# Optimization experiments

Hardware: AMD Instinct MI355X
Metric: run time of the kernel (lower is better)

Reference implementation:

```python
import jax, jax.numpy as jnp
import numpy as np

V, D, S, L, H = 32000, 768, 1024, 6, 12
HS = D // H
EPS = 1e-5


def setup_inputs() -> dict:
    key = jax.random.key(0)
    ks = jax.random.split(key, 20)
    std = 0.02
    inp = {
        "idx": jax.random.randint(ks[0], (4, 1024), 0, V),
        "tok_emb": jax.random.normal(ks[1], (V, D), jnp.float32) * std,
        "pos_emb": jax.random.normal(ks[2], (S, D), jnp.float32) * std,
        "Wq": jax.random.normal(ks[3], (L, H, D, HS), jnp.float32) * std,
        "Wk": jax.random.normal(ks[4], (L, H, D, HS), jnp.float32) * std,
        "Wv": jax.random.normal(ks[5], (L, H, D, HS), jnp.float32) * std,
        "Wp": jax.random.normal(ks[6], (L, D, D), jnp.float32) * std,
        "bp": jnp.zeros((L, D), jnp.float32),
        "ln1g": jnp.ones((L, D), jnp.float32),
        "ln1b": jnp.zeros((L, D), jnp.float32),
        "ln2g": jnp.ones((L, D), jnp.float32),
        "ln2b": jnp.zeros((L, D), jnp.float32),
        "W1": jax.random.normal(ks[7], (L, D, 4 * D), jnp.float32) * std,
        "b1": jnp.zeros((L, 4 * D), jnp.float32),
        "W2": jax.random.normal(ks[8], (L, 4 * D, D), jnp.float32) * std,
        "b2": jnp.zeros((L, D), jnp.float32),
        "lnfg": jnp.ones((D,), jnp.float32),
        "lnfb": jnp.zeros((D,), jnp.float32),
        "lmW": jax.random.normal(ks[9], (D, V), jnp.float32) * std,
        "lmb": jnp.zeros((V,), jnp.float32),
    }
    return inp


def _layernorm(x, g, b):
    m = jnp.mean(x, axis=-1, keepdims=True)
    v = jnp.mean(jnp.square(x - m), axis=-1, keepdims=True)
    return (x - m) * jax.lax.rsqrt(v + EPS) * g + b


def _gpt_forward(idx, tok_emb, pos_emb, Wq, Wk, Wv, Wp, bp,
                 ln1g, ln1b, ln2g, ln2b, W1, b1, W2, b2,
                 lnfg, lnfb, lmW, lmb):
    B, T = idx.shape
    x = tok_emb[idx] + pos_emb[:T]              # [B,T,D]
    tril = jnp.tril(jnp.ones((T, T), bool))
    scale = HS ** -0.5
    for l in range(L):
        h = _layernorm(x, ln1g[l], ln1b[l])
        q = jnp.einsum('btd,hdk->bhtk', h, Wq[l])
        k = jnp.einsum('btd,hdk->bhtk', h, Wk[l])
        v = jnp.einsum('btd,hdk->bhtk', h, Wv[l])
        att = jnp.einsum('bhtk,bhsk->bhts', q, k) * scale
        att = jnp.where(tril, att, -jnp.inf)
        att = jax.nn.softmax(att, axis=-1)
        o = jnp.einsum('bhts,bhsk->bhtk', att, v)          # [B,H,T,HS]
        o = o.transpose(0, 2, 1, 3).reshape(B, T, D)       # concat heads
        x = x + o @ Wp[l] + bp[l]
        h2 = _layernorm(x, ln2g[l], ln2b[l])
        x = x + jax.nn.relu(h2 @ W1[l] + b1[l]) @ W2[l] + b2[l]
    x = _layernorm(x, lnfg, lnfb)
    logits = x @ lmW + lmb                                  # [B,T,V]
    return logits


def reference(idx, tok_emb, pos_emb, Wq, Wk, Wv, Wp, bp,
              ln1g, ln1b, ln2g, ln2b, W1, b1, W2, b2,
              lnfg, lnfb, lmW, lmb):
    return _gpt_forward(idx, tok_emb, pos_emb, Wq, Wk, Wv, Wp, bp,
                        ln1g, ln1b, ln2g, ln2b, W1, b1, W2, b2,
                        lnfg, lnfb, lmW, lmb)
```

## Files before the change

### kernel.cpp

```cpp
#include <hip/hip_runtime.h>
#include <hip/hip_bf16.h>
#include <cstdint>
#include <cstddef>


typedef __bf16 bf16x8 __attribute__((ext_vector_type(8)));
typedef __bf16 bf16x4 __attribute__((ext_vector_type(4)));
typedef float  f32x4  __attribute__((ext_vector_type(4)));

#define MFMA16(a, b, c) __builtin_amdgcn_mfma_f32_16x16x32_bf16((a), (b), (c), 0, 0, 0)

__device__ __forceinline__ void g2l16(const void* g, void* l) {
    __builtin_amdgcn_global_load_lds(
        (const __attribute__((address_space(1))) void*)g,
        (__attribute__((address_space(3))) void*)l, 16, 0, 0);
}

__global__ __launch_bounds__(256) void transpose_cvt(
    const float* __restrict__ src, __bf16* __restrict__ dst,
    int K, int N, int nNT)
{
    const float* s = src + (size_t)blockIdx.y * K * N;
    __bf16*      d = dst + (size_t)blockIdx.y * K * N;
    int kt = blockIdx.x / nNT, nt = blockIdx.x % nNT;
    int k0 = kt * 32, n0 = nt * 32;
    __shared__ float t[32][33];
    int tx = threadIdx.x & 31, ty = threadIdx.x >> 5;
#pragma unroll
    for (int i = 0; i < 4; i++)
        t[ty + i * 8][tx] = s[(size_t)(k0 + ty + i * 8) * N + n0 + tx];
    __syncthreads();
#pragma unroll
    for (int i = 0; i < 4; i++)
        d[(size_t)(n0 + ty + i * 8) * K + k0 + tx] = (__bf16)t[tx][ty + i * 8];
}

__global__ __launch_bounds__(256) void repack_qkv(
    const float* __restrict__ Wq, const float* __restrict__ Wk,
    const float* __restrict__ Wv, __bf16* __restrict__ dst)
{
    int l = blockIdx.z;
    int m = blockIdx.y / 12, h = blockIdx.y % 12;
    int kt = blockIdx.x / 2, nt = blockIdx.x % 2;
    const float* W = (m == 0 ? Wq : (m == 1 ? Wk : Wv)) + ((size_t)(l * 12 + h)) * 768 * 64;
    __bf16* d = dst + (size_t)l * 2304 * 768 + (size_t)(m * 768 + h * 64) * 768;
    int k0 = kt * 32, n0 = nt * 32;
    __shared__ float t[32][33];
    int tx = threadIdx.x & 31, ty = threadIdx.x >> 5;
#pragma unroll
    for (int i = 0; i < 4; i++)
        t[ty + i * 8][tx] = W[(size_t)(k0 + ty + i * 8) * 64 + n0 + tx];
    __syncthreads();
#pragma unroll
    for (int i = 0; i < 4; i++)
        d[(size_t)(n0 + ty + i * 8) * 768 + k0 + tx] = (__bf16)t[tx][ty + i * 8];
}

__global__ __launch_bounds__(256) void embed_kernel(
    const int* __restrict__ idx, const float* __restrict__ tok,
    const float* __restrict__ pos, float* __restrict__ x)
{
    const int t = blockIdx.x, tid = threadIdx.x;
    int id = idx[t];
    const float* te = tok + (size_t)id * 768;
    const float* pe = pos + (size_t)(t & 1023) * 768;
    float* xr = x + (size_t)t * 768;
    xr[tid]       = te[tid]       + pe[tid];
    xr[tid + 256] = te[tid + 256] + pe[tid + 256];
    xr[tid + 512] = te[tid + 512] + pe[tid + 512];
}

__global__ __launch_bounds__(256) void ln_kernel(
    const float* __restrict__ x, const float* __restrict__ g,
    const float* __restrict__ bb, __bf16* __restrict__ out)
{
    const int row = blockIdx.x, tid = threadIdx.x;
    const float* xr = x + (size_t)row * 768;
    float v0 = xr[tid], v1 = xr[tid + 256], v2 = xr[tid + 512];
    float s  = v0 + v1 + v2;
    float s2 = v0 * v0 + v1 * v1 + v2 * v2;
#pragma unroll
    for (int d = 1; d < 64; d <<= 1) {
        s  += __shfl_xor(s, d);
        s2 += __shfl_xor(s2, d);
    }
    __shared__ float sb[8];
    int w = tid >> 6, l = tid & 63;
    if (l == 0) { sb[w] = s; sb[4 + w] = s2; }
    __syncthreads();
    s  = sb[0] + sb[1] + sb[2] + sb[3];
    s2 = sb[4] + sb[5] + sb[6] + sb[7];
    float mean = s * (1.f / 768.f);
    float var  = s2 * (1.f / 768.f) - mean * mean;
    float rstd = rsqrtf(var + 1e-5f);
    __bf16* orow = out + (size_t)row * 768;
    orow[tid]       = (__bf16)((v0 - mean) * rstd * g[tid]       + bb[tid]);
    orow[tid + 256] = (__bf16)((v1 - mean) * rstd * g[tid + 256] + bb[tid + 256]);
    orow[tid + 512] = (__bf16)((v2 - mean) * rstd * g[tid + 512] + bb[tid + 512]);
}

template <int RELU, int BIAS, int RES, int OBF16, int VT>
__global__ __launch_bounds__(256, 4) void gemm_bt(
    const __bf16* __restrict__ A, const __bf16* __restrict__ Bt,
    const float* __restrict__ bias, const float* __restrict__ res,
    void* __restrict__ Cout, __bf16* __restrict__ vt, int M, int N, int K)
{
    __shared__ __bf16 As[128 * 64];
    __shared__ __bf16 Bs[128 * 64];
    const int tid = threadIdx.x;
    const int w = tid >> 6, lane = tid & 63, lr = lane & 15, lg = lane >> 4;
    const int wr = w >> 1, wc = w & 1;

    const int MT  = gridDim.y;
    const int nwg = gridDim.x * gridDim.y;
    const int ord = blockIdx.y * gridDim.x + blockIdx.x;
    const int qq = nwg >> 3, rm = nwg & 7;
    const int xcd = ord & 7, pos = ord >> 3;
    const int wgid = (xcd < rm ? xcd * (qq + 1) : rm * (qq + 1) + (xcd - rm) * qq) + pos;
    const int m0 = (wgid % MT) * 128, n0 = (wgid / MT) * 128;

    f32x4 acc[4][4];
#pragma unroll
    for (int i = 0; i < 4; i++)
#pragma unroll
        for (int j = 0; j < 4; j++) acc[i][j] = (f32x4){0.f, 0.f, 0.f, 0.f};

    const __bf16* Abase = A  + (size_t)m0 * K;
    const __bf16* Bbase = Bt + (size_t)n0 * K;

    for (int k0 = 0; k0 < K; k0 += 64) {
#pragma unroll
        for (int u = 0; u < 4; ++u) {
            int chunk = u * 256 + tid;
            int rr = chunk >> 3, cc = chunk & 7;
            int se = (cc ^ (rr & 7)) << 3;
            g2l16(Abase + (size_t)rr * K + k0 + se, (char*)As + chunk * 16);
            g2l16(Bbase + (size_t)rr * K + k0 + se, (char*)Bs + chunk * 16);
        }
        __syncthreads();
#pragma unroll
        for (int ks = 0; ks < 2; ++ks) {
            bf16x8 af[4], bfv[4];
#pragma unroll
            for (int i = 0; i < 4; ++i) {
                int ra = wr * 64 + i * 16 + lr;
                af[i]  = *(const bf16x8*)((const char*)As + ra * 128 + (((ks * 4 + lg) ^ (ra & 7)) << 4));
                int rb = wc * 64 + i * 16 + lr;
                bfv[i] = *(const bf16x8*)((const char*)Bs + rb * 128 + (((ks * 4 + lg) ^ (rb & 7)) << 4));
            }
#pragma unroll
            for (int i = 0; i < 4; ++i)
#pragma unroll
                for (int j = 0; j < 4; ++j)
                    acc[i][j] = MFMA16(af[i], bfv[j], acc[i][j]);
        }
        __syncthreads();
    }

    const bool isv = VT && (n0 >= 1536);
#pragma unroll
    for (int i = 0; i < 4; i++) {
        int row = m0 + wr * 64 + i * 16 + lg * 4;
#pragma unroll
        for (int j = 0; j < 4; j++) {
            int col = n0 + wc * 64 + j * 16 + lr;
            if (isv) {
                int bb = row >> 10, tl = row & 1023;
                int vrow = (bb * 12 + ((col - 1536) >> 6)) * 64 + (col & 63);
                bf16x4 pv;
#pragma unroll
                for (int rr = 0; rr < 4; ++rr) pv[rr] = (__bf16)(acc[i][j][rr]);
                *(bf16x4*)&vt[(size_t)vrow * 1024 + tl] = pv;
            } else {
                float bv = BIAS ? bias[col] : 0.f;
#pragma unroll
                for (int rr = 0; rr < 4; rr++) {
                    float v = acc[i][j][rr] + bv;
                    if (RES)  v += res[(size_t)(row + rr) * N + col];
                    if (RELU) v = fmaxf(v, 0.f);
                    if (OBF16) ((__bf16*)Cout)[(size_t)(row + rr) * N + col] = (__bf16)v;
                    else       ((float*)Cout)[(size_t)(row + rr) * N + col] = v;
                }
            }
        }
    }
}

__global__ __launch_bounds__(256, 3) void attn_kernel(
    const __bf16* __restrict__ qkv, const __bf16* __restrict__ vt,
    __bf16* __restrict__ o)
{
    __shared__ __bf16 Kl[128 * 64];
    __shared__ __bf16 Vl[64 * 128];
    __shared__ __bf16 Pl[4][16][72];
    const int qb = blockIdx.x, h = blockIdx.y, b = blockIdx.z;
    const int tid = threadIdx.x, w = tid >> 6, lane = tid & 63, lr = lane & 15, lg = lane >> 4;
    const int q0 = qb * 64 + w * 16;
    const size_t rowb = (size_t)b * 1024;
    const __bf16* Kg = qkv + rowb * 2304 + 768 + (size_t)h * 64;
    const __bf16* Vg = vt + (size_t)(b * 12 + h) * 64 * 1024;

    bf16x8 qf[2];
    {
        const __bf16* qp = qkv + (rowb + q0 + lr) * 2304 + h * 64 + lg * 8;
        qf[0] = *(const bf16x8*)qp;
        qf[1] = *(const bf16x8*)(qp + 32);
    }

    f32x4 oacc[4];
#pragma unroll
    for (int i = 0; i < 4; i++) oacc[i] = (f32x4){0.f, 0.f, 0.f, 0.f};
    float lpart[4] = {0.f, 0.f, 0.f, 0.f};

    const int nkb = (qb >> 1) + 1;
    for (int kb = 0; kb < nkb; ++kb) {
        __syncthreads();
#pragma unroll
        for (int u = 0; u < 4; ++u) {
            int chunk = u * 256 + tid;
            int kr = chunk >> 3, cc = chunk & 7;
            g2l16(Kg + (size_t)(kb * 128 + kr) * 2304 + ((cc ^ (kr & 7)) << 3),
                  (char*)Kl + chunk * 16);
        }
#pragma unroll
        for (int u = 0; u < 4; ++u) {
            int chunk = u * 256 + tid;
            int vr = chunk >> 4, cc = chunk & 15;
            g2l16(Vg + (size_t)vr * 1024 + kb * 128 + ((cc ^ (vr & 15)) << 3),
                  (char*)Vl + chunk * 16);
        }
        __syncthreads();

#pragma unroll
        for (int hh = 0; hh < 2; ++hh) {
            if (kb * 128 + hh * 64 > q0 + 15) break;
            float e[4][4];
#pragma unroll
            for (int cb = 0; cb < 4; ++cb) {
                const int krow = hh * 64 + cb * 16 + lr;
                const int key  = kb * 128 + krow;
                bf16x8 k0 = *(const bf16x8*)((const char*)Kl + krow * 128 + ((lg ^ (krow & 7)) << 4));
                bf16x8 k1 = *(const bf16x8*)((const char*)Kl + krow * 128 + (((4 + lg) ^ (krow & 7)) << 4));
                f32x4 s = (f32x4){0.f, 0.f, 0.f, 0.f};
                s = MFMA16(qf[0], k0, s);
                s = MFMA16(qf[1], k1, s);
#pragma unroll
                for (int rr = 0; rr < 4; rr++) {
                    int qrow = q0 + lg * 4 + rr;
                    float p = (key > qrow) ? -1e30f : s[rr] * 0.125f;
                    e[cb][rr] = __expf(p - 3.0f);
                }
            }
#pragma unroll
            for (int rr = 0; rr < 4; rr++) {
                lpart[rr] += (e[0][rr] + e[1][rr]) + (e[2][rr] + e[3][rr]);
                Pl[w][lg * 4 + rr][lr]      = (__bf16)e[0][rr];
                Pl[w][lg * 4 + rr][16 + lr] = (__bf16)e[1][rr];
                Pl[w][lg * 4 + rr][32 + lr] = (__bf16)e[2][rr];
                Pl[w][lg * 4 + rr][48 + lr] = (__bf16)e[3][rr];
            }
            bf16x8 pf0 = *(const bf16x8*)&Pl[w][lr][lg * 8];
            bf16x8 pf1 = *(const bf16x8*)&Pl[w][lr][32 + lg * 8];
#pragma unroll
            for (int nb = 0; nb < 4; nb++) {
                const int vrow = nb * 16 + lr;
                bf16x8 v0 = *(const bf16x8*)((const char*)Vl + vrow * 256 + (((hh * 8 + lg) ^ (vrow & 15)) << 4));
                bf16x8 v1 = *(const bf16x8*)((const char*)Vl + vrow * 256 + (((hh * 8 + 4 + lg) ^ (vrow & 15)) << 4));
                oacc[nb] = MFMA16(pf0, v0, oacc[nb]);
                oacc[nb] = MFMA16(pf1, v1, oacc[nb]);
            }
        }
    }

#pragma unroll
    for (int rr = 0; rr < 4; rr++) {
        float ls = lpart[rr];
        ls += __shfl_xor(ls, 1);
        ls += __shfl_xor(ls, 2);
        ls += __shfl_xor(ls, 4);
        ls += __shfl_xor(ls, 8);
        float inv = 1.0f / ls;
        size_t row = rowb + q0 + lg * 4 + rr;
#pragma unroll
        for (int nb = 0; nb < 4; nb++)
            o[row * 768 + h * 64 + nb * 16 + lr] = (__bf16)(oacc[nb][rr] * inv);
    }
}

extern "C" void kernel_launch(void* const* d_in, const int* in_sizes, int n_in,
                              void* d_out, int out_size, void* d_ws, size_t ws_size,
                              hipStream_t stream)
{
    (void)in_sizes; (void)n_in; (void)out_size; (void)ws_size;
    const int*   idx  = (const int*)d_in[0];
    const float* tok  = (const float*)d_in[1];
    const float* pos  = (const float*)d_in[2];
    const float* Wq   = (const float*)d_in[3];
    const float* Wk   = (const float*)d_in[4];
    const float* Wv   = (const float*)d_in[5];
    const float* Wp   = (const float*)d_in[6];
    const float* bp   = (const float*)d_in[7];
    const float* ln1g = (const float*)d_in[8];
    const float* ln1b = (const float*)d_in[9];
    const float* ln2g = (const float*)d_in[10];
    const float* ln2b = (const float*)d_in[11];
    const float* W1   = (const float*)d_in[12];
    const float* b1   = (const float*)d_in[13];
    const float* W2   = (const float*)d_in[14];
    const float* b2   = (const float*)d_in[15];
    const float* lnfg = (const float*)d_in[16];
    const float* lnfb = (const float*)d_in[17];
    const float* lmW  = (const float*)d_in[18];
    const float* lmb  = (const float*)d_in[19];

    char* ws = (char*)d_ws;
    size_t off = 0;
    auto alloc = [&](size_t bytes) {
        char* p = ws + off;
        off += (bytes + 255) & ~(size_t)255;
        return p;
    };
    __bf16* Wqkv_t = (__bf16*)alloc((size_t)6 * 2304 * 768 * 2);
    __bf16* Wp_t   = (__bf16*)alloc((size_t)6 * 768 * 768 * 2);
    __bf16* W1_t   = (__bf16*)alloc((size_t)6 * 3072 * 768 * 2);
    __bf16* W2_t   = (__bf16*)alloc((size_t)6 * 768 * 3072 * 2);
    __bf16* lm_t   = (__bf16*)alloc((size_t)32000 * 768 * 2);
    float*  x      = (float*)alloc((size_t)4096 * 768 * 4);
    __bf16* hbuf   = (__bf16*)alloc((size_t)4096 * 768 * 2);
    __bf16* qkv    = (__bf16*)alloc((size_t)4096 * 2304 * 2);
    __bf16* obuf   = (__bf16*)alloc((size_t)4096 * 768 * 2);
    __bf16* mlp    = (__bf16*)alloc((size_t)4096 * 3072 * 2);
    __bf16* vt     = mlp;

    transpose_cvt<<<dim3(24 * 24, 6), 256, 0, stream>>>(Wp, Wp_t, 768, 768, 24);
    transpose_cvt<<<dim3(24 * 96, 6), 256, 0, stream>>>(W1, W1_t, 768, 3072, 96);
    transpose_cvt<<<dim3(96 * 24, 6), 256, 0, stream>>>(W2, W2_t, 3072, 768, 24);
    transpose_cvt<<<dim3(24 * 1000, 1), 256, 0, stream>>>(lmW, lm_t, 768, 32000, 1000);
    repack_qkv<<<dim3(48, 36, 6), 256, 0, stream>>>(Wq, Wk, Wv, Wqkv_t);

    embed_kernel<<<4096, 256, 0, stream>>>(idx, tok, pos, x);

    for (int l = 0; l < 6; l++) {
        ln_kernel<<<4096, 256, 0, stream>>>(x, ln1g + l * 768, ln1b + l * 768, hbuf);
        gemm_bt<0, 0, 0, 1, 1><<<dim3(18, 32), 256, 0, stream>>>(
            hbuf, Wqkv_t + (size_t)l * 2304 * 768, nullptr, nullptr, qkv, vt, 4096, 2304, 768);
        attn_kernel<<<dim3(16, 12, 4), 256, 0, stream>>>(qkv, vt, obuf);
        gemm_bt<0, 1, 1, 0, 0><<<dim3(6, 32), 256, 0, stream>>>(
            obuf, Wp_t + (size_t)l * 768 * 768, bp + l * 768, x, x, nullptr, 4096, 768, 768);
        ln_kernel<<<4096, 256, 0, stream>>>(x, ln2g + l * 768, ln2b + l * 768, hbuf);
        gemm_bt<1, 1, 0, 1, 0><<<dim3(24, 32), 256, 0, stream>>>(
            hbuf, W1_t + (size_t)l * 3072 * 768, b1 + l * 3072, nullptr, mlp, nullptr, 4096, 3072, 768);
        gemm_bt<0, 1, 1, 0, 0><<<dim3(6, 32), 256, 0, stream>>>(
            mlp, W2_t + (size_t)l * 768 * 3072, b2 + l * 768, x, x, nullptr, 4096, 768, 3072);
    }

    ln_kernel<<<4096, 256, 0, stream>>>(x, lnfg, lnfb, hbuf);
    gemm_bt<0, 1, 0, 0, 0><<<dim3(250, 32), 256, 0, stream>>>(
        hbuf, lm_t, lmb, nullptr, d_out, nullptr, 4096, 32000, 768);
}
```

Measured before the change: 1.512 ms.

## Vectorize transposes/embed/layernorm and add 256x128-tile LM-head GEMM

The weight transpose and repack kernels now read float4 and write bf16x4. Embedding and layernorm process one row per wavefront with vectorized loads, which removes the shared-memory reduction and barrier in layernorm. A new 512-thread LM-head GEMM uses 256x128 tiles with 8 waves, doubling A-tile reuse for the largest matmul. The larger tiles raise LDS and register use per block, which may reduce occupancy.

```diff
diff --git a/kernel.cpp b/kernel.cpp
--- a/kernel.cpp
+++ b/kernel.cpp
@@ -25,14 +25,15 @@
     int kt = blockIdx.x / nNT, nt = blockIdx.x % nNT;
     int k0 = kt * 32, n0 = nt * 32;
     __shared__ float t[32][33];
-    int tx = threadIdx.x & 31, ty = threadIdx.x >> 5;
-#pragma unroll
-    for (int i = 0; i < 4; i++)
-        t[ty + i * 8][tx] = s[(size_t)(k0 + ty + i * 8) * N + n0 + tx];
+    int rr = threadIdx.x >> 3, c4 = (threadIdx.x & 7) * 4;
+    f32x4 v = *(const f32x4*)&s[(size_t)(k0 + rr) * N + n0 + c4];
+#pragma unroll
+    for (int j = 0; j < 4; j++) t[rr][c4 + j] = v[j];
     __syncthreads();
-#pragma unroll
-    for (int i = 0; i < 4; i++)
-        d[(size_t)(n0 + ty + i * 8) * K + k0 + tx] = (__bf16)t[tx][ty + i * 8];
+    bf16x4 ov;
+#pragma unroll
+    for (int j = 0; j < 4; j++) ov[j] = (__bf16)t[c4 + j][rr];
+    *(bf16x4*)&d[(size_t)(n0 + rr) * K + k0 + c4] = ov;
 }
 
 __global__ __launch_bounds__(256) void repack_qkv(
@@ -46,57 +47,72 @@
     __bf16* d = dst + (size_t)l * 2304 * 768 + (size_t)(m * 768 + h * 64) * 768;
     int k0 = kt * 32, n0 = nt * 32;
     __shared__ float t[32][33];
-    int tx = threadIdx.x & 31, ty = threadIdx.x >> 5;
-#pragma unroll
-    for (int i = 0; i < 4; i++)
-        t[ty + i * 8][tx] = W[(size_t)(k0 + ty + i * 8) * 64 + n0 + tx];
+    int rr = threadIdx.x >> 3, c4 = (threadIdx.x & 7) * 4;
+    f32x4 v = *(const f32x4*)&W[(size_t)(k0 + rr) * 64 + n0 + c4];
+#pragma unroll
+    for (int j = 0; j < 4; j++) t[rr][c4 + j] = v[j];
     __syncthreads();
-#pragma unroll
-    for (int i = 0; i < 4; i++)
-        d[(size_t)(n0 + ty + i * 8) * 768 + k0 + tx] = (__bf16)t[tx][ty + i * 8];
+    bf16x4 ov;
+#pragma unroll
+    for (int j = 0; j < 4; j++) ov[j] = (__bf16)t[c4 + j][rr];
+    *(bf16x4*)&d[(size_t)(n0 + rr) * 768 + k0 + c4] = ov;
 }
 
 __global__ __launch_bounds__(256) void embed_kernel(
     const int* __restrict__ idx, const float* __restrict__ tok,
     const float* __restrict__ pos, float* __restrict__ x)
 {
-    const int t = blockIdx.x, tid = threadIdx.x;
-    int id = idx[t];
+    const int row = blockIdx.x * 4 + (threadIdx.x >> 6);
+    const int lane = threadIdx.x & 63;
+    int id = idx[row];
     const float* te = tok + (size_t)id * 768;
-    const float* pe = pos + (size_t)(t & 1023) * 768;
-    float* xr = x + (size_t)t * 768;
-    xr[tid]       = te[tid]       + pe[tid];
-    xr[tid + 256] = te[tid + 256] + pe[tid + 256];
-    xr[tid + 512] = te[tid + 512] + pe[tid + 512];
+    const float* pe = pos + (size_t)(row & 1023) * 768;
+    float* xr = x + (size_t)row * 768;
+#pragma unroll
+    for (int p = 0; p < 3; p++) {
+        int c = p * 256 + lane * 4;
+        f32x4 a = *(const f32x4*)&te[c];
+        f32x4 b = *(const f32x4*)&pe[c];
+        a[0] += b[0]; a[1] += b[1]; a[2] += b[2]; a[3] += b[3];
+        *(f32x4*)&xr[c] = a;
+    }
 }
 
 __global__ __launch_bounds__(256) void ln_kernel(
     const float* __restrict__ x, const float* __restrict__ g,
     const float* __restrict__ bb, __bf16* __restrict__ out)
 {
-    const int row = blockIdx.x, tid = threadIdx.x;
+    const int row = blockIdx.x * 4 + (threadIdx.x >> 6);
+    const int lane = threadIdx.x & 63;
     const float* xr = x + (size_t)row * 768;
-    float v0 = xr[tid], v1 = xr[tid + 256], v2 = xr[tid + 512];
-    float s  = v0 + v1 + v2;
-    float s2 = v0 * v0 + v1 * v1 + v2 * v2;
+    f32x4 v[3];
+    float s = 0.f, s2 = 0.f;
+#pragma unroll
+    for (int p = 0; p < 3; p++) {
+        v[p] = *(const f32x4*)&xr[p * 256 + lane * 4];
+#pragma unroll
+        for (int j = 0; j < 4; j++) { s += v[p][j]; s2 += v[p][j] * v[p][j]; }
+    }
 #pragma unroll
     for (int d = 1; d < 64; d <<= 1) {
         s  += __shfl_xor(s, d);
         s2 += __shfl_xor(s2, d);
     }
-    __shared__ float sb[8];
-    int w = tid >> 6, l = tid & 63;
-    if (l == 0) { sb[w] = s; sb[4 + w] = s2; }
-    __syncthreads();
-    s  = sb[0] + sb[1] + sb[2] + sb[3];
-    s2 = sb[4] + sb[5] + sb[6] + sb[7];
     float mean = s * (1.f / 768.f);
     float var  = s2 * (1.f / 768.f) - mean * mean;
     float rstd = rsqrtf(var + 1e-5f);
     __bf16* orow = out + (size_t)row * 768;
-    orow[tid]       = (__bf16)((v0 - mean) * rstd * g[tid]       + bb[tid]);
-    orow[tid + 256] = (__bf16)((v1 - mean) * rstd * g[tid + 256] + bb[tid + 256]);
-    orow[tid + 512] = (__bf16)((v2 - mean) * rstd * g[tid + 512] + bb[tid + 512]);
+#pragma unroll
+    for (int p = 0; p < 3; p++) {
+        int c = p * 256 + lane * 4;
+        f32x4 gg = *(const f32x4*)&g[c];
+        f32x4 bv = *(const f32x4*)&bb[c];
+        bf16x4 ov;
+#pragma unroll
+        for (int j = 0; j < 4; j++)
+            ov[j] = (__bf16)((v[p][j] - mean) * rstd * gg[j] + bv[j]);
+        *(bf16x4*)&orow[c] = ov;
+    }
 }
 
 template <int RELU, int BIAS, int RES, int OBF16, int VT>
@@ -182,6 +198,83 @@
                     else       ((float*)Cout)[(size_t)(row + rr) * N + col] = v;
                 }
             }
+        }
+    }
+}
+
+template <int BIAS>
+__global__ __launch_bounds__(512, 4) void gemm_lm(
+    const __bf16* __restrict__ A, const __bf16* __restrict__ Bt,
+    const float* __restrict__ bias, float* __restrict__ C, int M, int N, int K)
+{
+    __shared__ __bf16 As[256 * 64];
+    __shared__ __bf16 Bs[128 * 64];
+    const int tid = threadIdx.x;
+    const int w = tid >> 6, lane = tid & 63, lr = lane & 15, lg = lane >> 4;
+    const int wm = w >> 1, wn = w & 1;
+
+    const int MT  = gridDim.y;
+    const int nwg = gridDim.x * gridDim.y;
+    const int ord = blockIdx.y * gridDim.x + blockIdx.x;
+    const int qq = nwg >> 3, rm = nwg & 7;
+    const int xcd = ord & 7, pos = ord >> 3;
+    const int wgid = (xcd < rm ? xcd * (qq + 1) : rm * (qq + 1) + (xcd - rm) * qq) + pos;
+    const int m0 = (wgid % MT) * 256, n0 = (wgid / MT) * 128;
+
+    f32x4 acc[4][4];
+#pragma unroll
+    for (int i = 0; i < 4; i++)
+#pragma unroll
+        for (int j = 0; j < 4; j++) acc[i][j] = (f32x4){0.f, 0.f, 0.f, 0.f};
+
+    const __bf16* Abase = A  + (size_t)m0 * K;
+    const __bf16* Bbase = Bt + (size_t)n0 * K;
+
+    for (int k0 = 0; k0 < K; k0 += 64) {
+#pragma unroll
+        for (int u = 0; u < 4; ++u) {
+            int chunk = u * 512 + tid;
+            int rr = chunk >> 3, cc = chunk & 7;
+            g2l16(Abase + (size_t)rr * K + k0 + ((cc ^ (rr & 7)) << 3),
+                  (char*)As + chunk * 16);
+        }
+#pragma unroll
+        for (int u = 0; u < 2; ++u) {
+            int chunk = u * 512 + tid;
+            int rr = chunk >> 3, cc = chunk & 7;
+            g2l16(Bbase + (size_t)rr * K + k0 + ((cc ^ (rr & 7)) << 3),
+                  (char*)Bs + chunk * 16);
+        }
+        __syncthreads();
+#pragma unroll
+        for (int ks = 0; ks < 2; ++ks) {
+            bf16x8 af[4], bfv[4];
+#pragma unroll
+            for (int i = 0; i < 4; ++i) {
+                int ra = wm * 64 + i * 16 + lr;
+                af[i]  = *(const bf16x8*)((const char*)As + ra * 128 + (((ks * 4 + lg) ^ (ra & 7)) << 4));
+                int rb = wn * 64 + i * 16 + lr;
+                bfv[i] = *(const bf16x8*)((const char*)Bs + rb * 128 + (((ks * 4 + lg) ^ (rb & 7)) << 4));
+            }
+#pragma unroll
+            for (int i = 0; i < 4; ++i)
+#pragma unroll
+                for (int j = 0; j < 4; ++j)
+                    acc[i][j] = MFMA16(af[i], bfv[j], acc[i][j]);
+        }
+        __syncthreads();
+    }
+
+#pragma unroll
+    for (int i = 0; i < 4; i++) {
+        int row = m0 + wm * 64 + i * 16 + lg * 4;
+#pragma unroll
+        for (int j = 0; j < 4; j++) {
+            int col = n0 + wn * 64 + j * 16 + lr;
+            float bv = BIAS ? bias[col] : 0.f;
+#pragma unroll
+            for (int rr = 0; rr < 4; rr++)
+                C[(size_t)(row + rr) * N + col] = acc[i][j][rr] + bv;
         }
     }
 }
@@ -338,23 +431,23 @@
     transpose_cvt<<<dim3(24 * 1000, 1), 256, 0, stream>>>(lmW, lm_t, 768, 32000, 1000);
     repack_qkv<<<dim3(48, 36, 6), 256, 0, stream>>>(Wq, Wk, Wv, Wqkv_t);
 
-    embed_kernel<<<4096, 256, 0, stream>>>(idx, tok, pos, x);
+    embed_kernel<<<1024, 256, 0, stream>>>(idx, tok, pos, x);
 
     for (int l = 0; l < 6; l++) {
-        ln_kernel<<<4096, 256, 0, stream>>>(x, ln1g + l * 768, ln1b + l * 768, hbuf);
+        ln_kernel<<<1024, 256, 0, stream>>>(x, ln1g + l * 768, ln1b + l * 768, hbuf);
         gemm_bt<0, 0, 0, 1, 1><<<dim3(18, 32), 256, 0, stream>>>(
             hbuf, Wqkv_t + (size_t)l * 2304 * 768, nullptr, nullptr, qkv, vt, 4096, 2304, 768);
         attn_kernel<<<dim3(16, 12, 4), 256, 0, stream>>>(qkv, vt, obuf);
         gemm_bt<0, 1, 1, 0, 0><<<dim3(6, 32), 256, 0, stream>>>(
             obuf, Wp_t + (size_t)l * 768 * 768, bp + l * 768, x, x, nullptr, 4096, 768, 768);
-        ln_kernel<<<4096, 256, 0, stream>>>(x, ln2g + l * 768, ln2b + l * 768, hbuf);
+        ln_kernel<<<1024, 256, 0, stream>>>(x, ln2g + l * 768, ln2b + l * 768, hbuf);
         gemm_bt<1, 1, 0, 1, 0><<<dim3(24, 32), 256, 0, stream>>>(
             hbuf, W1_t + (size_t)l * 3072 * 768, b1 + l * 3072, nullptr, mlp, nullptr, 4096, 3072, 768);
         gemm_bt<0, 1, 1, 0, 0><<<dim3(6, 32), 256, 0, stream>>>(
             mlp, W2_t + (size_t)l * 768 * 3072, b2 + l * 768, x, x, nullptr, 4096, 768, 3072);
     }
 
-    ln_kernel<<<4096, 256, 0, stream>>>(x, lnfg, lnfb, hbuf);
-    gemm_bt<0, 1, 0, 0, 0><<<dim3(250, 32), 256, 0, stream>>>(
-        hbuf, lm_t, lmb, nullptr, d_out, nullptr, 4096, 32000, 768);
-}
+    ln_kernel<<<1024, 256, 0, stream>>>(x, lnfg, lnfb, hbuf);
+    gemm_lm<1><<<dim3(250, 16), 512, 0, stream>>>(
+        hbuf, lm_t, lmb, (float*)d_out, 4096, 32000, 768);
+}
```

Result: no change. 1.489 ms (-1.6%).
